# Optimization experiments

Hardware: AMD Instinct MI355X
Metric: run time of the kernel (lower is better)

Reference implementation:

```python
import jax, jax.numpy as jnp
import numpy as np

DN = ('NHWC', 'HWIO', 'NHWC')


def setup_inputs() -> dict:
    key = jax.random.key(0)
    ks = jax.random.split(key, 5)
    B, H, W, C = 2, 256, 256, 192
    heads = 4
    x = jax.random.normal(ks[0], (B, H, W, C), dtype=jnp.float32)
    w_qkv = jax.random.normal(ks[1], (1, 1, C, 3 * C), dtype=jnp.float32) * 0.05
    b_qkv = jnp.zeros((3 * C,), dtype=jnp.float32)
    w_dw = jax.random.normal(ks[2], (3, 3, 1, 3 * C), dtype=jnp.float32) * 0.05
    b_dw = jnp.zeros((3 * C,), dtype=jnp.float32)
    temperature = jnp.ones((1, heads, 1, 1), dtype=jnp.float32)
    w_out = jax.random.normal(ks[3], (1, 1, C, C), dtype=jnp.float32) * 0.05
    b_out = jnp.zeros((C,), dtype=jnp.float32)
    return {"x": x, "w_qkv": w_qkv, "b_qkv": b_qkv, "w_dw": w_dw,
            "b_dw": b_dw, "temperature": temperature, "w_out": w_out,
            "b_out": b_out}


def _mdta(x, w_qkv, b_qkv, w_dw, b_dw, temperature, w_out, b_out):
    B, H, W, C = x.shape
    heads = temperature.shape[1]
    c = C // heads  # per-head channels
    # 1x1 pointwise qkv projection -> [B,H,W,3C]
    qkv = jax.lax.conv_general_dilated(x, w_qkv, (1, 1), 'SAME',
                                       dimension_numbers=DN) + b_qkv
    # 3x3 depthwise conv (groups = 3C)
    qkv = jax.lax.conv_general_dilated(qkv, w_dw, (1, 1), 'SAME',
                                       dimension_numbers=DN,
                                       feature_group_count=3 * C) + b_dw
    q, k, v = jnp.split(qkv, 3, axis=-1)  # each [B,H,W,C]

    def to_heads(t):
        # [B,H,W,C] -> [B, heads, c, HW]
        return t.reshape(B, H * W, heads, c).transpose(0, 2, 3, 1)

    q, k, v = to_heads(q), to_heads(k), to_heads(v)
    # L2-normalize along the spatial (HW) axis
    q = q / jnp.maximum(jnp.linalg.norm(q, axis=-1, keepdims=True), 1e-12)
    k = k / jnp.maximum(jnp.linalg.norm(k, axis=-1, keepdims=True), 1e-12)
    # channel-wise transposed attention: [B,heads,c,c]
    attn = jnp.einsum('bhcn,bhdn->bhcd', q, k) * temperature
    attn = jax.nn.softmax(attn, axis=-1)
    out = jnp.einsum('bhcd,bhdn->bhcn', attn, v)  # [B,heads,c,HW]
    out = out.transpose(0, 3, 1, 2).reshape(B, H, W, C)
    # output 1x1 projection
    out = jax.lax.conv_general_dilated(out, w_out, (1, 1), 'SAME',
                                       dimension_numbers=DN) + b_out
    return out


def reference(x, w_qkv, b_qkv, w_dw, b_dw, temperature, w_out, b_out):
    return _mdta(x, w_qkv, b_qkv, w_dw, b_dw, temperature, w_out, b_out)
```

## Files before the change

### kernel.cpp

```cpp
#include <hip/hip_runtime.h>

typedef unsigned short ushort_t;
typedef __attribute__((ext_vector_type(8))) short short8;
typedef __attribute__((ext_vector_type(4))) float f32x4;

#define B_ 2
#define HW_ 65536
#define MTOT_ 131072
#define C_ 192
#define C3_ 576
#define HEADS_ 4
#define CH_ 48

#define OFF_QKV0  ((size_t)0)
#define OFF_QKV1  ((size_t)150994944)
#define OFF_XB    OFF_QKV1
#define OFF_P     OFF_QKV0
#define OFF_BT    ((size_t)301989888)
#define OFF_S     ((size_t)302211072)
#define OFF_NQ    ((size_t)302284800)
#define OFF_NK    ((size_t)302286336)
#define OFF_ATTN  ((size_t)302287872)
#define OFF_MT    ((size_t)302361600)

__device__ __forceinline__ float b2f(ushort_t u) {
    unsigned v = ((unsigned)u) << 16;
    return __builtin_bit_cast(float, v);
}
__device__ __forceinline__ ushort_t f2b(float f) {
    unsigned u = __builtin_bit_cast(unsigned, f);
    u = (u + 0x7fffu + ((u >> 16) & 1u)) >> 16;
    return (ushort_t)u;
}
__device__ __forceinline__ void storev(float* p, float v) { *p = v; }
__device__ __forceinline__ void storev(ushort_t* p, float v) { *p = f2b(v); }

__global__ void k_cvt_x(const float* __restrict__ x, ushort_t* __restrict__ xb) {
    int i = (blockIdx.x * 256 + threadIdx.x) * 8;
    float4 a = *(const float4*)(x + i);
    float4 b = *(const float4*)(x + i + 4);
    ushort_t o[8];
    o[0] = f2b(a.x); o[1] = f2b(a.y); o[2] = f2b(a.z); o[3] = f2b(a.w);
    o[4] = f2b(b.x); o[5] = f2b(b.y); o[6] = f2b(b.z); o[7] = f2b(b.w);
    *(uint4*)(xb + i) = *(uint4*)o;
}

__global__ void k0_transpose(const float* __restrict__ w, ushort_t* __restrict__ bt) {
    int idx = blockIdx.x * 256 + threadIdx.x;
    int n = idx / 192, k = idx - n * 192;
    bt[idx] = f2b(w[k * 576 + n]);
}

template <typename OutT>
__global__ __launch_bounds__(256) void gemm_k192(
    const ushort_t* __restrict__ A, int lda, int acol0,
    const ushort_t* __restrict__ BT, int bstride,
    const float* __restrict__ bias,
    OutT* __restrict__ Cout, int ldc)
{
    const int m0 = blockIdx.y * 64;
    const int n0 = blockIdx.x * 64;
    const ushort_t* bt = BT + (bstride ? (size_t)(m0 >> 16) * (size_t)bstride : 0);

    __shared__ ushort_t As[64 * 72];
    __shared__ ushort_t Bs[64 * 72];

    const int t = threadIdx.x;
    const int wave = t >> 6, lane = t & 63;
    const int quad = lane >> 4, l15 = lane & 15;
    const int wm = (wave >> 1) * 32, wn = (wave & 1) * 32;
    const int srow = t >> 2, scol = (t & 3) * 16;

    f32x4 acc[2][2] = {};

    for (int kk = 0; kk < 192; kk += 64) {
        const ushort_t* ga = A + (size_t)(m0 + srow) * lda + acol0 + kk + scol;
        uint4 va0 = *(const uint4*)ga;
        uint4 va1 = *(const uint4*)(ga + 8);
        const ushort_t* gb = bt + (size_t)(n0 + srow) * 192 + kk + scol;
        uint4 vb0 = *(const uint4*)gb;
        uint4 vb1 = *(const uint4*)(gb + 8);
        *(uint4*)&As[srow * 72 + scol] = va0;
        *(uint4*)&As[srow * 72 + scol + 8] = va1;
        *(uint4*)&Bs[srow * 72 + scol] = vb0;
        *(uint4*)&Bs[srow * 72 + scol + 8] = vb1;
        __syncthreads();
#pragma unroll
        for (int ks = 0; ks < 2; ks++) {
            short8 a0 = *(const short8*)&As[(wm + l15) * 72 + ks * 32 + quad * 8];
            short8 a1 = *(const short8*)&As[(wm + 16 + l15) * 72 + ks * 32 + quad * 8];
            short8 b0 = *(const short8*)&Bs[(wn + l15) * 72 + ks * 32 + quad * 8];
            short8 b1 = *(const short8*)&Bs[(wn + 16 + l15) * 72 + ks * 32 + quad * 8];
            acc[0][0] = __builtin_amdgcn_mfma_f32_16x16x32_bf16(a0, b0, acc[0][0], 0, 0, 0);
            acc[0][1] = __builtin_amdgcn_mfma_f32_16x16x32_bf16(a0, b1, acc[0][1], 0, 0, 0);
            acc[1][0] = __builtin_amdgcn_mfma_f32_16x16x32_bf16(a1, b0, acc[1][0], 0, 0, 0);
            acc[1][1] = __builtin_amdgcn_mfma_f32_16x16x32_bf16(a1, b1, acc[1][1], 0, 0, 0);
        }
        __syncthreads();
    }
#pragma unroll
    for (int sm = 0; sm < 2; sm++) {
#pragma unroll
        for (int sn = 0; sn < 2; sn++) {
            int col = n0 + wn + sn * 16 + l15;
            float bv = bias ? bias[col] : 0.f;
#pragma unroll
            for (int r = 0; r < 4; r++) {
                int row = m0 + wm + sm * 16 + quad * 4 + r;
                storev(&Cout[(size_t)row * ldc + col], acc[sm][sn][r] + bv);
            }
        }
    }
}

#define R_STRIP 16

__global__ __launch_bounds__(256) void k2_dwconv(const ushort_t* __restrict__ qkv0,
        const float* __restrict__ wdw, const float* __restrict__ bdw,
        ushort_t* __restrict__ qkv1)
{
    const int tid = blockIdx.x * 256 + threadIdx.x;
    const int c8 = tid % 72;
    const int t1 = tid / 72;
    const int x  = t1 & 255;
    const int t2 = t1 >> 8;
    const int s  = t2 & 15;
    const int b  = t2 >> 4;
    const int y0 = s * R_STRIP;
    const int cbase = c8 * 8;

    const bool xm = (x > 0), xp = (x < 255);
    const ushort_t* colbase = qkv0 + ((size_t)(b * HW_ + x) * C3_ + cbase);
    ushort_t*       ocol    = qkv1 + ((size_t)(b * HW_ + x) * C3_ + cbase);
    const size_t rstride = (size_t)256 * C3_;

    float w[3][3][8], bw[8];
#pragma unroll
    for (int ky = 0; ky < 3; ++ky)
#pragma unroll
        for (int kx = 0; kx < 3; ++kx) {
            const float* wp = wdw + ((ky * 3 + kx) * C3_ + cbase);
            float4 lo = *(const float4*)wp;
            float4 hi = *(const float4*)(wp + 4);
            w[ky][kx][0] = lo.x; w[ky][kx][1] = lo.y; w[ky][kx][2] = lo.z; w[ky][kx][3] = lo.w;
            w[ky][kx][4] = hi.x; w[ky][kx][5] = hi.y; w[ky][kx][6] = hi.z; w[ky][kx][7] = hi.w;
        }
    {
        float4 lo = *(const float4*)(bdw + cbase);
        float4 hi = *(const float4*)(bdw + cbase + 4);
        bw[0] = lo.x; bw[1] = lo.y; bw[2] = lo.z; bw[3] = lo.w;
        bw[4] = hi.x; bw[5] = hi.y; bw[6] = hi.z; bw[7] = hi.w;
    }

    const uint4 z4 = make_uint4(0, 0, 0, 0);
    auto loadrow = [&](int r, uint4& d0, uint4& d1, uint4& d2) {
        if ((unsigned)r <= 255u) {
            const ushort_t* p = colbase + (size_t)r * rstride;
            d1 = *(const uint4*)p;
            d0 = xm ? *(const uint4*)(p - C3_) : z4;
            d2 = xp ? *(const uint4*)(p + C3_) : z4;
        } else { d0 = z4; d1 = z4; d2 = z4; }
    };

    float A[3][8] = {};
    uint4 c0, c1, c2;
    loadrow(y0 - 1, c0, c1, c2);

#pragma unroll
    for (int RR = 0; RR < R_STRIP + 2; ++RR) {
        const int r = y0 - 1 + RR;
        uint4 n0 = z4, n1 = z4, n2 = z4;
        if (RR < R_STRIP + 1) loadrow(r + 1, n0, n1, n2);

        float rf[3][8];
        {
            const ushort_t* dd = (const ushort_t*)&c0;
#pragma unroll
            for (int j = 0; j < 8; ++j) rf[0][j] = b2f(dd[j]);
            dd = (const ushort_t*)&c1;
#pragma unroll
            for (int j = 0; j < 8; ++j) rf[1][j] = b2f(dd[j]);
            dd = (const ushort_t*)&c2;
#pragma unroll
            for (int j = 0; j < 8; ++j) rf[2][j] = b2f(dd[j]);
        }

        if (RR >= 1 && RR <= R_STRIP) {
#pragma unroll
            for (int kx = 0; kx < 3; ++kx)
#pragma unroll
                for (int j = 0; j < 8; ++j)
                    A[RR % 3][j] = fmaf(rf[kx][j], w[1][kx][j], A[RR % 3][j]);
        }
        if (RR <= R_STRIP - 1) {
#pragma unroll
            for (int kx = 0; kx < 3; ++kx)
#pragma unroll
                for (int j = 0; j < 8; ++j)
                    A[(RR + 1) % 3][j] = fmaf(rf[kx][j], w[0][kx][j], A[(RR + 1) % 3][j]);
        }
        if (RR >= 2) {
#pragma unroll
            for (int kx = 0; kx < 3; ++kx)
#pragma unroll
                for (int j = 0; j < 8; ++j)
                    A[(RR + 2) % 3][j] = fmaf(rf[kx][j], w[2][kx][j], A[(RR + 2) % 3][j]);
            ushort_t ov[8];
#pragma unroll
            for (int j = 0; j < 8; ++j) {
                ov[j] = f2b(A[(RR + 2) % 3][j] + bw[j]);
                A[(RR + 2) % 3][j] = 0.f;
            }
            *(uint4*)(ocol + (size_t)(r - 1) * rstride) = *(uint4*)ov;
        }
        c0 = n0; c1 = n1; c2 = n2;
    }
}

#define GR_LDSSTRIDE 136

__global__ __launch_bounds__(256) void k3_gram_mfma(const ushort_t* __restrict__ qkv1,
        float* __restrict__ P)
{
    const int bh = blockIdx.y;
    const int b = bh >> 2, h = bh & 3;
    const int slice = blockIdx.x;
    const int t = threadIdx.x;
    const int wave = t >> 6, lane = t & 63;
    const int quad = lane >> 4, l15 = lane & 15;

    __shared__ float red[7680];
    ushort_t* Z = (ushort_t*)red;

    f32x4 acc[15] = {};
    const ushort_t* basep = qkv1 + (size_t)(b * HW_) * C3_;
    const int row = t & 127;
    const int seghalf = t >> 7;

    for (int tile = 0; tile < 8; ++tile) {
        const int nbase = slice * 1024 + tile * 128;
        uint4 u[6];
#pragma unroll
        for (int k = 0; k < 6; ++k) {
            int seg = k * 2 + seghalf;
            int cg = (seg < 6) ? (h * CH_ + seg * 8) : (C_ + h * CH_ + (seg - 6) * 8);
            u[k] = *(const uint4*)(basep + (size_t)(nbase + row) * C3_ + cg);
        }
        __syncthreads();
#pragma unroll
        for (int k = 0; k < 6; ++k) {
            int seg = k * 2 + seghalf;
            int zc = seg * 8;
            const ushort_t* dd = (const ushort_t*)&u[k];
#pragma unroll
            for (int j = 0; j < 8; ++j)
                Z[(zc + j) * GR_LDSSTRIDE + row] = dd[j];
        }
        __syncthreads();
        const int n0 = wave * 32 + quad * 8;
        short8 F[6];
#pragma unroll
        for (int c = 0; c < 6; ++c)
            F[c] = *(const short8*)&Z[(c * 16 + l15) * GR_LDSSTRIDE + n0];
#pragma unroll
        for (int i = 0; i < 3; ++i)
#pragma unroll
            for (int j = 0; j < 3; ++j)
                acc[i * 3 + j] = __builtin_amdgcn_mfma_f32_16x16x32_bf16(F[i], F[3 + j], acc[i * 3 + j], 0, 0, 0);
#pragma unroll
        for (int i = 0; i < 3; ++i) {
            acc[9 + i]  = __builtin_amdgcn_mfma_f32_16x16x32_bf16(F[i], F[i], acc[9 + i], 0, 0, 0);
            acc[12 + i] = __builtin_amdgcn_mfma_f32_16x16x32_bf16(F[3 + i], F[3 + i], acc[12 + i], 0, 0, 0);
        }
    }

    __syncthreads();
    if (wave & 1) {
        float* dst = red + (wave >> 1) * (15 * 256);
#pragma unroll
        for (int tt = 0; tt < 15; ++tt)
            *(f32x4*)&dst[tt * 256 + lane * 4] = acc[tt];
    }
    __syncthreads();
    if (!(wave & 1)) {
        const float* src = red + (wave >> 1) * (15 * 256);
        const int sp = slice * 2 + (wave >> 1);
#pragma unroll
        for (int tt = 0; tt < 15; ++tt) {
            f32x4 v = *(const f32x4*)&src[tt * 256 + lane * 4];
#pragma unroll
            for (int r = 0; r < 4; ++r) {
                int e = (quad * 4 + r) * 16 + l15;
                P[(((size_t)bh * 15 + tt) * 128 + sp) * 256 + e] = acc[tt][r] + v[r];
            }
        }
    }
}

__global__ __launch_bounds__(256) void k3r_reduce(const float* __restrict__ P,
        float* __restrict__ S, float* __restrict__ NQ, float* __restrict__ NK)
{
    int idx = blockIdx.x * 256 + threadIdx.x;
    int bh = idx / 3840;
    int rem = idx - bh * 3840;
    int tt = rem >> 8;
    int e = rem & 255;
    const float* p = P + (((size_t)bh * 15 + tt) * 128) * 256 + e;
    float s = 0.f;
#pragma unroll 8
    for (int sp = 0; sp < 128; ++sp) s += p[(size_t)sp * 256];
    int r = e >> 4, c = e & 15;
    if (tt < 9) {
        int i = tt / 3, j = tt - i * 3;
        S[bh * 2304 + (i * 16 + r) * 48 + j * 16 + c] = s;
    } else if (tt < 12) {
        if (r == c) NQ[bh * 48 + (tt - 9) * 16 + r] = s;
    } else {
        if (r == c) NK[bh * 48 + (tt - 12) * 16 + r] = s;
    }
}

__global__ void k4a_softmax(const float* __restrict__ S, const float* __restrict__ NQ,
                            const float* __restrict__ NK, const float* __restrict__ temp,
                            float* __restrict__ ATT)
{
    int bh = blockIdx.y, cq = blockIdx.x;
    int h = bh & 3;
    int t = threadIdx.x;
    float nq = fmaxf(sqrtf(NQ[bh * 48 + cq]), 1e-12f);
    float tv = temp[h];
    float logit = -1e30f;
    if (t < 48) {
        float nk = fmaxf(sqrtf(NK[bh * 48 + t]), 1e-12f);
        logit = S[bh * 2304 + cq * 48 + t] * tv / (nq * nk);
    }
    float m = logit;
    for (int o = 32; o > 0; o >>= 1) m = fmaxf(m, __shfl_xor(m, o));
    float e = (t < 48) ? __expf(logit - m) : 0.f;
    float ssum = e;
    for (int o = 32; o > 0; o >>= 1) ssum += __shfl_xor(ssum, o);
    if (t < 48) ATT[bh * 2304 + cq * 48 + t] = e / ssum;
}

__global__ void k4b_buildM(const float* __restrict__ ATT, const float* __restrict__ wout,
                           ushort_t* __restrict__ MT)
{
    int idx = blockIdx.x * 256 + threadIdx.x;
    int b = idx / 36864; int rem = idx - b * 36864;
    int j = rem / 192;   int d = rem - j * 192;
    int h = d / 48, dd = d - h * 48;
    const float* ap = ATT + (size_t)(b * 4 + h) * 2304 + dd;
    const float* wp = wout + (size_t)(h * 48) * 192 + j;
    float s = 0.f;
#pragma unroll 8
    for (int cq = 0; cq < 48; cq++) s += ap[cq * 48] * wp[cq * 192];
    MT[idx] = f2b(s);
}

extern "C" void kernel_launch(void* const* d_in, const int* in_sizes, int n_in,
                              void* d_out, int out_size, void* d_ws, size_t ws_size,
                              hipStream_t stream) {
    const float* x     = (const float*)d_in[0];
    const float* w_qkv = (const float*)d_in[1];
    const float* b_qkv = (const float*)d_in[2];
    const float* w_dw  = (const float*)d_in[3];
    const float* b_dw  = (const float*)d_in[4];
    const float* temp  = (const float*)d_in[5];
    const float* w_out = (const float*)d_in[6];
    const float* b_out = (const float*)d_in[7];
    float* out = (float*)d_out;

    char* ws = (char*)d_ws;
    ushort_t* qkv0 = (ushort_t*)(ws + OFF_QKV0);
    ushort_t* qkv1 = (ushort_t*)(ws + OFF_QKV1);
    ushort_t* xb   = (ushort_t*)(ws + OFF_XB);
    float*    Pb   = (float*)(ws + OFF_P);
    ushort_t* btq  = (ushort_t*)(ws + OFF_BT);
    float*    Sb   = (float*)(ws + OFF_S);
    float*    NQ   = (float*)(ws + OFF_NQ);
    float*    NK   = (float*)(ws + OFF_NK);
    float*    ATT  = (float*)(ws + OFF_ATTN);
    ushort_t* MT   = (ushort_t*)(ws + OFF_MT);

    k_cvt_x<<<12288, 256, 0, stream>>>(x, xb);
    k0_transpose<<<432, 256, 0, stream>>>(w_qkv, btq);
    gemm_k192<ushort_t><<<dim3(9, 2048), 256, 0, stream>>>(xb, 192, 0, btq, 0, b_qkv, qkv0, 576);
    k2_dwconv<<<2304, 256, 0, stream>>>(qkv0, w_dw, b_dw, qkv1);
    k3_gram_mfma<<<dim3(64, 8), 256, 0, stream>>>(qkv1, Pb);
    k3r_reduce<<<120, 256, 0, stream>>>(Pb, Sb, NQ, NK);
    k4a_softmax<<<dim3(48, 8), 64, 0, stream>>>(Sb, NQ, NK, temp, ATT);
    k4b_buildM<<<288, 256, 0, stream>>>(ATT, w_out, MT);
    gemm_k192<float><<<dim3(3, 2048), 256, 0, stream>>>(qkv1, 576, 384, MT, 36864, b_out, out, 192);
}
```

Baseline: 449.1 us.

## Fuse fp32-to-bf16 input conversion into QKV GEMM and narrow dwconv channel vectors

Removes the separate x conversion kernel: the QKV GEMM now loads fp32 x directly and converts to bf16 while staging into shared memory. This drops one full read and write pass over x. Since the GEMM grid has 9 column blocks, each x row tile is re-read and converted 9 times, as fp32 at twice the bytes. Separately, the depthwise conv now handles 4 channels per thread instead of 8, doubling the thread count to raise parallelism, at the cost of narrower 8-byte memory accesses.

Result: slower. 484.7 us (+7.9%).

```diff
diff --git a/kernel.cpp b/kernel.cpp
--- a/kernel.cpp
+++ b/kernel.cpp
@@ -14,7 +14,6 @@
 
 #define OFF_QKV0  ((size_t)0)
 #define OFF_QKV1  ((size_t)150994944)
-#define OFF_XB    OFF_QKV1
 #define OFF_P     OFF_QKV0
 #define OFF_BT    ((size_t)301989888)
 #define OFF_S     ((size_t)302211072)
@@ -35,14 +34,21 @@
 __device__ __forceinline__ void storev(float* p, float v) { *p = v; }
 __device__ __forceinline__ void storev(ushort_t* p, float v) { *p = f2b(v); }
 
-__global__ void k_cvt_x(const float* __restrict__ x, ushort_t* __restrict__ xb) {
-    int i = (blockIdx.x * 256 + threadIdx.x) * 8;
-    float4 a = *(const float4*)(x + i);
-    float4 b = *(const float4*)(x + i + 4);
-    ushort_t o[8];
-    o[0] = f2b(a.x); o[1] = f2b(a.y); o[2] = f2b(a.z); o[3] = f2b(a.w);
-    o[4] = f2b(b.x); o[5] = f2b(b.y); o[6] = f2b(b.z); o[7] = f2b(b.w);
-    *(uint4*)(xb + i) = *(uint4*)o;
+__device__ __forceinline__ void load16(const ushort_t* p, uint4& lo, uint4& hi) {
+    lo = *(const uint4*)p;
+    hi = *(const uint4*)(p + 8);
+}
+__device__ __forceinline__ void load16(const float* p, uint4& lo, uint4& hi) {
+    float4 a = *(const float4*)p;
+    float4 b = *(const float4*)(p + 4);
+    float4 c = *(const float4*)(p + 8);
+    float4 d = *(const float4*)(p + 12);
+    ushort_t o[16];
+    o[0]=f2b(a.x); o[1]=f2b(a.y); o[2]=f2b(a.z); o[3]=f2b(a.w);
+    o[4]=f2b(b.x); o[5]=f2b(b.y); o[6]=f2b(b.z); o[7]=f2b(b.w);
+    o[8]=f2b(c.x); o[9]=f2b(c.y); o[10]=f2b(c.z); o[11]=f2b(c.w);
+    o[12]=f2b(d.x); o[13]=f2b(d.y); o[14]=f2b(d.z); o[15]=f2b(d.w);
+    lo = *(uint4*)o; hi = *(uint4*)(o + 8);
 }
 
 __global__ void k0_transpose(const float* __restrict__ w, ushort_t* __restrict__ bt) {
@@ -51,9 +57,9 @@
     bt[idx] = f2b(w[k * 576 + n]);
 }
 
-template <typename OutT>
+template <typename AT, typename OutT>
 __global__ __launch_bounds__(256) void gemm_k192(
-    const ushort_t* __restrict__ A, int lda, int acol0,
+    const AT* __restrict__ A, int lda, int acol0,
     const ushort_t* __restrict__ BT, int bstride,
     const float* __restrict__ bias,
     OutT* __restrict__ Cout, int ldc)
@@ -74,9 +80,9 @@
     f32x4 acc[2][2] = {};
 
     for (int kk = 0; kk < 192; kk += 64) {
-        const ushort_t* ga = A + (size_t)(m0 + srow) * lda + acol0 + kk + scol;
-        uint4 va0 = *(const uint4*)ga;
-        uint4 va1 = *(const uint4*)(ga + 8);
+        const AT* ga = A + (size_t)(m0 + srow) * lda + acol0 + kk + scol;
+        uint4 va0, va1;
+        load16(ga, va0, va1);
         const ushort_t* gb = bt + (size_t)(n0 + srow) * 192 + kk + scol;
         uint4 vb0 = *(const uint4*)gb;
         uint4 vb1 = *(const uint4*)(gb + 8);
@@ -120,98 +126,93 @@
         ushort_t* __restrict__ qkv1)
 {
     const int tid = blockIdx.x * 256 + threadIdx.x;
-    const int c8 = tid % 72;
-    const int t1 = tid / 72;
+    const int c4 = tid % 144;
+    const int t1 = tid / 144;
     const int x  = t1 & 255;
     const int t2 = t1 >> 8;
     const int s  = t2 & 15;
     const int b  = t2 >> 4;
     const int y0 = s * R_STRIP;
-    const int cbase = c8 * 8;
+    const int cbase = c4 * 4;
 
     const bool xm = (x > 0), xp = (x < 255);
     const ushort_t* colbase = qkv0 + ((size_t)(b * HW_ + x) * C3_ + cbase);
     ushort_t*       ocol    = qkv1 + ((size_t)(b * HW_ + x) * C3_ + cbase);
     const size_t rstride = (size_t)256 * C3_;
 
-    float w[3][3][8], bw[8];
+    float w[3][3][4], bw[4];
 #pragma unroll
     for (int ky = 0; ky < 3; ++ky)
 #pragma unroll
         for (int kx = 0; kx < 3; ++kx) {
-            const float* wp = wdw + ((ky * 3 + kx) * C3_ + cbase);
-            float4 lo = *(const float4*)wp;
-            float4 hi = *(const float4*)(wp + 4);
-            w[ky][kx][0] = lo.x; w[ky][kx][1] = lo.y; w[ky][kx][2] = lo.z; w[ky][kx][3] = lo.w;
-            w[ky][kx][4] = hi.x; w[ky][kx][5] = hi.y; w[ky][kx][6] = hi.z; w[ky][kx][7] = hi.w;
+            float4 wv = *(const float4*)(wdw + ((ky * 3 + kx) * C3_ + cbase));
+            w[ky][kx][0] = wv.x; w[ky][kx][1] = wv.y; w[ky][kx][2] = wv.z; w[ky][kx][3] = wv.w;
         }
     {
-        float4 lo = *(const float4*)(bdw + cbase);
-        float4 hi = *(const float4*)(bdw + cbase + 4);
-        bw[0] = lo.x; bw[1] = lo.y; bw[2] = lo.z; bw[3] = lo.w;
-        bw[4] = hi.x; bw[5] = hi.y; bw[6] = hi.z; bw[7] = hi.w;
-    }
-
-    const uint4 z4 = make_uint4(0, 0, 0, 0);
-    auto loadrow = [&](int r, uint4& d0, uint4& d1, uint4& d2) {
+        float4 bv = *(const float4*)(bdw + cbase);
+        bw[0] = bv.x; bw[1] = bv.y; bw[2] = bv.z; bw[3] = bv.w;
+    }
+
+    const uint2 z2 = make_uint2(0, 0);
+    auto loadrow = [&](int r, uint2& d0, uint2& d1, uint2& d2) {
         if ((unsigned)r <= 255u) {
             const ushort_t* p = colbase + (size_t)r * rstride;
-            d1 = *(const uint4*)p;
-            d0 = xm ? *(const uint4*)(p - C3_) : z4;
-            d2 = xp ? *(const uint4*)(p + C3_) : z4;
-        } else { d0 = z4; d1 = z4; d2 = z4; }
+            d1 = *(const uint2*)p;
+            d0 = xm ? *(const uint2*)(p - C3_) : z2;
+            d2 = xp ? *(const uint2*)(p + C3_) : z2;
+        } else { d0 = z2; d1 = z2; d2 = z2; }
     };
 
-    float A[3][8] = {};
-    uint4 c0, c1, c2;
+    float A[3][4] = {};
+    uint2 c0, c1, c2;
     loadrow(y0 - 1, c0, c1, c2);
 
 #pragma unroll
     for (int RR = 0; RR < R_STRIP + 2; ++RR) {
         const int r = y0 - 1 + RR;
-        uint4 n0 = z4, n1 = z4, n2 = z4;
+        uint2 n0 = z2, n1 = z2, n2 = z2;
         if (RR < R_STRIP + 1) loadrow(r + 1, n0, n1, n2);
 
-        float rf[3][8];
+        float rf[3][4];
         {
             const ushort_t* dd = (const ushort_t*)&c0;
 #pragma unroll
-            for (int j = 0; j < 8; ++j) rf[0][j] = b2f(dd[j]);
+            for (int j = 0; j < 4; ++j) rf[0][j] = b2f(dd[j]);
             dd = (const ushort_t*)&c1;
 #pragma unroll
-            for (int j = 0; j < 8; ++j) rf[1][j] = b2f(dd[j]);
+            for (int j = 0; j < 4; ++j) rf[1][j] = b2f(dd[j]);
             dd = (const ushort_t*)&c2;
 #pragma unroll
-            for (int j = 0; j < 8; ++j) rf[2][j] = b2f(dd[j]);
+            for (int j = 0; j < 4; ++j) rf[2][j] = b2f(dd[j]);
         }
 
         if (RR >= 1 && RR <= R_STRIP) {
 #pragma unroll
             for (int kx = 0; kx < 3; ++kx)
 #pragma unroll
-                for (int j = 0; j < 8; ++j)
+                for (int j = 0; j < 4; ++j)
                     A[RR % 3][j] = fmaf(rf[kx][j], w[1][kx][j], A[RR % 3][j]);
         }
         if (RR <= R_STRIP - 1) {
 #pragma unroll
             for (int kx = 0; kx < 3; ++kx)
 #pragma unroll
-                for (int j = 0; j < 8; ++j)
+                for (int j = 0; j < 4; ++j)
                     A[(RR + 1) % 3][j] = fmaf(rf[kx][j], w[0][kx][j], A[(RR + 1) % 3][j]);
         }
         if (RR >= 2) {
 #pragma unroll
             for (int kx = 0; kx < 3; ++kx)
 #pragma unroll
-                for (int j = 0; j < 8; ++j)
+                for (int j = 0; j < 4; ++j)
                     A[(RR + 2) % 3][j] = fmaf(rf[kx][j], w[2][kx][j], A[(RR + 2) % 3][j]);
-            ushort_t ov[8];
-#pragma unroll
-            for (int j = 0; j < 8; ++j) {
+            ushort_t ov[4];
+#pragma unroll
+            for (int j = 0; j < 4; ++j) {
                 ov[j] = f2b(A[(RR + 2) % 3][j] + bw[j]);
                 A[(RR + 2) % 3][j] = 0.f;
             }
-            *(uint4*)(ocol + (size_t)(r - 1) * rstride) = *(uint4*)ov;
+            *(uint2*)(ocol + (size_t)(r - 1) * rstride) = *(uint2*)ov;
         }
         c0 = n0; c1 = n1; c2 = n2;
     }
@@ -373,7 +374,6 @@
     char* ws = (char*)d_ws;
     ushort_t* qkv0 = (ushort_t*)(ws + OFF_QKV0);
     ushort_t* qkv1 = (ushort_t*)(ws + OFF_QKV1);
-    ushort_t* xb   = (ushort_t*)(ws + OFF_XB);
     float*    Pb   = (float*)(ws + OFF_P);
     ushort_t* btq  = (ushort_t*)(ws + OFF_BT);
     float*    Sb   = (float*)(ws + OFF_S);
@@ -382,13 +382,12 @@
     float*    ATT  = (float*)(ws + OFF_ATTN);
     ushort_t* MT   = (ushort_t*)(ws + OFF_MT);
 
-    k_cvt_x<<<12288, 256, 0, stream>>>(x, xb);
     k0_transpose<<<432, 256, 0, stream>>>(w_qkv, btq);
-    gemm_k192<ushort_t><<<dim3(9, 2048), 256, 0, stream>>>(xb, 192, 0, btq, 0, b_qkv, qkv0, 576);
-    k2_dwconv<<<2304, 256, 0, stream>>>(qkv0, w_dw, b_dw, qkv1);
+    gemm_k192<float, ushort_t><<<dim3(9, 2048), 256, 0, stream>>>(x, 192, 0, btq, 0, b_qkv, qkv0, 576);
+    k2_dwconv<<<4608, 256, 0, stream>>>(qkv0, w_dw, b_dw, qkv1);
     k3_gram_mfma<<<dim3(64, 8), 256, 0, stream>>>(qkv1, Pb);
     k3r_reduce<<<120, 256, 0, stream>>>(Pb, Sb, NQ, NK);
     k4a_softmax<<<dim3(48, 8), 64, 0, stream>>>(Sb, NQ, NK, temp, ATT);
     k4b_buildM<<<288, 256, 0, stream>>>(ATT, w_out, MT);
-    gemm_k192<float><<<dim3(3, 2048), 256, 0, stream>>>(qkv1, 576, 384, MT, 36864, b_out, out, 192);
-}
+    gemm_k192<ushort_t, float><<<dim3(3, 2048), 256, 0, stream>>>(qkv1, 576, 384, MT, 36864, b_out, out, 192);
+}
```
